# Kernel tuning notes

Measured on AMD Instinct MI355X. Metric: run time of the kernel, lower is better.

Reference implementation:

```python
import jax, jax.numpy as jnp
import numpy as np

B, T, U, N, K, H, O = 64, 800, 64, 64, 10, 512, 121
CLIP_LSTM, CLIP_OUT = 10.0, 100.0


def setup_inputs() -> dict:
    key = jax.random.key(0)
    ks = jax.random.split(key, 16)
    s = 0.08
    return {
        "strokes": jax.random.normal(ks[0], (B, T, 3), jnp.float32),
        "transcriptions": jax.random.uniform(ks[1], (B, U, N), jnp.float32),
        "W0": jax.random.normal(ks[2], (3 + N, 4 * H), jnp.float32) * s,
        "R0": jax.random.normal(ks[3], (H, 4 * H), jnp.float32) * s,
        "b0": jnp.zeros((4 * H,), jnp.float32),
        "Wd": jax.random.normal(ks[4], (H, 3 * K), jnp.float32) * 0.01,
        "bd": jnp.zeros((3 * K,), jnp.float32),
        "W1": jax.random.normal(ks[5], (H + N + 3, 4 * H), jnp.float32) * s,
        "R1": jax.random.normal(ks[6], (H, 4 * H), jnp.float32) * s,
        "b1": jnp.zeros((4 * H,), jnp.float32),
        "W2": jax.random.normal(ks[7], (H + N + 3, 4 * H), jnp.float32) * s,
        "R2": jax.random.normal(ks[8], (H, 4 * H), jnp.float32) * s,
        "b2": jnp.zeros((4 * H,), jnp.float32),
        "Wo": jax.random.normal(ks[9], (3 * H, O), jnp.float32) * s,
        "bo": jnp.zeros((O,), jnp.float32),
    }


def _lstm_step(h, c, z):
    i, f, g, o = jnp.split(z, 4, axis=-1)
    c2 = jax.nn.sigmoid(f) * c + jax.nn.sigmoid(i) * jnp.tanh(g)
    h2 = jax.nn.sigmoid(o) * jnp.tanh(c2)
    return h2, c2


def _lstm_layer(x_seq, W, R, b):
    # x_seq: [T, B, D] -> hidden sequence [T, B, H]
    xz = jnp.einsum('tbd,dh->tbh', x_seq, W) + b  # precompute input projections

    def step(carry, xz_t):
        h, c = carry
        h2, c2 = _lstm_step(h, c, xz_t + h @ R)
        return (h2, c2), h2

    z0 = jnp.zeros((x_seq.shape[1], R.shape[0]), x_seq.dtype)
    _, hs = jax.lax.scan(step, (z0, z0), xz)
    return hs


def _make_clipper(cv):
    @jax.custom_vjp
    def f(y):
        return y
    f.defvjp(lambda y: (y, None), lambda _, dy: (jnp.clip(dy, -cv, cv),))
    return f


_clip_lstm = _make_clipper(CLIP_LSTM)
_clip_out = _make_clipper(CLIP_OUT)


def _forward(strokes, transcriptions, W0, R0, b0, Wd, bd, W1, R1, b1, W2, R2, b2, Wo, bo):
    idx = jnp.arange(1, U + 2, dtype=strokes.dtype)  # enumerated char positions [U+1]
    x_t = jnp.swapaxes(strokes, 0, 1)  # [T, B, 3]

    def step(carry, x):
        w, kappa, h, c = carry
        z = jnp.concatenate([x, w], axis=-1) @ W0 + h @ R0 + b0
        h2, c2 = _lstm_step(h, c, z)
        y = jnp.exp(h2 @ Wd + bd).reshape(-1, 3, K)  # [B, 3, K]
        alpha, beta, dk = y[:, 0], y[:, 1], y[:, 2]
        kappa2 = kappa + dk  # [B, K]
        # Gaussian window over U+1 positions, summed over K mixtures
        phi = alpha[..., None] * jnp.exp(-beta[..., None] * (kappa2[..., None] - idx) ** 2)
        wfull = phi.sum(axis=1)  # [B, U+1]
        att = jnp.argmax(wfull, axis=-1).astype(strokes.dtype)  # [B]
        w2 = jnp.einsum('bu,bun->bn', wfull[:, :U], transcriptions)  # soft window [B, N]
        return (w2, kappa2, h2, c2), (h2, w2, att)

    zf = lambda d: jnp.zeros((B, d), strokes.dtype)
    init = (zf(N), zf(K), zf(H), zf(H))
    _, (h0_seq, w_seq, att_seq) = jax.lax.scan(step, init, x_t)

    x1 = jnp.concatenate([_clip_lstm(h0_seq), w_seq, x_t], axis=-1)  # [T, B, H+N+3]
    h1_seq = _lstm_layer(x1, W1, R1, b1)
    x2 = jnp.concatenate([_clip_lstm(h1_seq), w_seq, x_t], axis=-1)
    h2_seq = _lstm_layer(x2, W2, R2, b2)
    hall = jnp.concatenate([h0_seq, h1_seq, h2_seq], axis=-1)  # [T, B, 3H]
    out = _clip_out(hall @ Wo + bo)
    return jnp.swapaxes(out, 0, 1), jnp.swapaxes(att_seq, 0, 1)  # [B,T,O], [B,T]


def reference(strokes, transcriptions, W0, R0, b0, Wd, bd, W1, R1, b1, W2, R2, b2, Wo, bo):
    return _forward(strokes, transcriptions, W0, R0, b0, Wd, bd, W1, R1, b1, W2, R2, b2, Wo, bo)
```

## Files before the change

### kernel.cpp

```cpp
#include <hip/hip_runtime.h>

#define B_   64
#define T_   800
#define U_   64
#define N_   64
#define KMIX 10
#define H_   512
#define O_   121
#define C4_  2048

#define NB_L0  64
#define NB_L1  64
#define NB_L2  64
#define NB_OUT 8
#define NB_ATT 8
#define NBLK  (NB_L0 + NB_L1 + NB_L2 + NB_OUT + NB_ATT)
#define NTHR  1024
#define RING  8
#define RB    (RING - 1)
#define FS    8

#define AL(pp) __hip_atomic_load((pp), __ATOMIC_RELAXED, __HIP_MEMORY_SCOPE_AGENT)

typedef float vf4 __attribute__((ext_vector_type(4)));

struct Params {
  const float* strokes; const float* transcr;
  const float* transcrT;
  const float* W0; const float* b0;
  const float* bd;
  const float* W1; const float* b1;
  const float* W2; const float* b2;
  const float* bo;
  const float4* PR0; const float4* PW0w;
  const float4* PH1; const float4* PR1; const float4* PW1w;
  const float4* PH2; const float4* PR2; const float4* PW2w;
  const float4* PWo; const float4* PWd;
  float* h0r; float* h1r; float* h2r;
  float* wr;
  int *h0f, *h1f, *h2f, *wfl, *outf;
  float* outp; float* attp;
};

__device__ __forceinline__ float sigf(float x) { return 1.0f / (1.0f + expf(-x)); }

__device__ __forceinline__ double f32q(double x) {
  double ax = fabs(x);
  if (ax >= 0x1p-126) return (double)(float)x;
  return rint(x * 0x1p149) * 0x1p-149;
}

__device__ __forceinline__ void cstoref(float* p, float v) {
  __hip_atomic_store(p, v, __ATOMIC_RELAXED, __HIP_MEMORY_SCOPE_AGENT);
}

__device__ __forceinline__ vf4 cld1(const void* p0) {
  vf4 a;
  asm volatile("global_load_dwordx4 %0, %1, off sc0 sc1\n\t"
               "s_waitcnt vmcnt(0)"
               : "=&v"(a) : "v"(p0) : "memory");
  return a;
}
__device__ __forceinline__ void cld2(const void* p0, const void* p1, vf4& a, vf4& b) {
  asm volatile("global_load_dwordx4 %0, %2, off sc0 sc1\n\t"
               "global_load_dwordx4 %1, %3, off sc0 sc1\n\t"
               "s_waitcnt vmcnt(0)"
               : "=&v"(a), "=&v"(b) : "v"(p0), "v"(p1) : "memory");
}
__device__ __forceinline__ void cld3(const void* p0, const void* p1, const void* p2,
                                     vf4& a, vf4& b, vf4& c) {
  asm volatile("global_load_dwordx4 %0, %3, off sc0 sc1\n\t"
               "global_load_dwordx4 %1, %4, off sc0 sc1\n\t"
               "global_load_dwordx4 %2, %5, off sc0 sc1\n\t"
               "s_waitcnt vmcnt(0)"
               : "=&v"(a), "=&v"(b), "=&v"(c)
               : "v"(p0), "v"(p1), "v"(p2) : "memory");
}

__device__ __forceinline__ int* FP(int* arr, int tt, int bq) {
  return arr + ((size_t)tt * 8 + bq) * FS;
}
__device__ __forceinline__ void waitflag(const int* f, int target) {
  while (__hip_atomic_load(f, __ATOMIC_RELAXED, __HIP_MEMORY_SCOPE_AGENT) < target)
    __builtin_amdgcn_s_sleep(1);
}
__device__ __forceinline__ void postflag(int* f) {
  __hip_atomic_fetch_add(f, 1, __ATOMIC_RELAXED, __HIP_MEMORY_SCOPE_AGENT);
}

__device__ __forceinline__ void stage4k(float* dstL, const float* src, int t) {
  vf4 v = cld1((const vf4*)src + t);
  *((vf4*)dstL + t) = v;
}
__device__ __forceinline__ void stage4k2(float* d1, const float* s1,
                                         float* d2, const float* s2, int t) {
  vf4 a, b;
  cld2((const vf4*)s1 + t, (const vf4*)s2 + t, a, b);
  *((vf4*)d1 + t) = a;
  *((vf4*)d2 + t) = b;
}
__device__ __forceinline__ void stage512(float* dstL, const float* src, int t) {
  if (t < 128) {
    vf4 v = cld1((const vf4*)src + t);
    *((vf4*)dstL + t) = v;
  }
}

__device__ __forceinline__ void dot4gl(const float* Xl,
                                       const float4* __restrict__ W,
                                       int k4, int col, float acc[4]) {
  const float4* X = (const float4*)Xl;
  #pragma unroll 2
  for (int kk = 0; kk < k4; ++kk) {
    float4 xv = X[kk];
    #pragma unroll
    for (int g = 0; g < 4; ++g) {
      float4 wv = W[kk * C4_ + g * H_ + col];
      acc[g] = fmaf(xv.x, wv.x, acc[g]);
      acc[g] = fmaf(xv.y, wv.y, acc[g]);
      acc[g] = fmaf(xv.z, wv.z, acc[g]);
      acc[g] = fmaf(xv.w, wv.w, acc[g]);
    }
  }
}

__device__ __forceinline__ float dot1l(const float* Xl,
                                       const float4* __restrict__ W,
                                       int k4, int stride) {
  const float4* X = (const float4*)Xl;
  float a = 0.0f;
  #pragma unroll 4
  for (int kk = 0; kk < k4; ++kk) {
    float4 xv = X[kk];
    float4 wv = W[kk * stride];
    a = fmaf(xv.x, wv.x, a); a = fmaf(xv.y, wv.y, a);
    a = fmaf(xv.z, wv.z, a); a = fmaf(xv.w, wv.w, a);
  }
  return a;
}

__global__ void pack_k(const float* __restrict__ src, float* __restrict__ dst,
                       int K, int C, int ld) {
  int idx = blockIdx.x * 256 + threadIdx.x;
  if (idx >= K * C) return;
  int k = idx / C, c = idx - k * C;
  dst[(size_t)(k >> 2) * C * 4 + (size_t)c * 4 + (k & 3)] = src[(size_t)k * ld + c];
}

__global__ void pack_t(const float* __restrict__ src, float* __restrict__ dst) {
  int idx = blockIdx.x * 256 + threadIdx.x;
  if (idx >= B_ * U_ * N_) return;
  int b = idx >> 12, r = idx & 4095;
  int u = r >> 6, n = r & 63;
  dst[((size_t)b * N_ + n) * U_ + u] = src[((size_t)b * U_ + u) * N_ + n];
}

__global__ __launch_bounds__(NTHR, 4)
void net_kernel(Params p) {
  const int q = blockIdx.x;
  const int t = threadIdx.x;

  __shared__ float  s_buf[12288];
  __shared__ float  s_y[16][32];
  __shared__ float  s_k2[16][10];
  __shared__ float  s_kap[16][10];
  __shared__ double s_wf[16][66];

  if (q < NB_L0) {
    const int bq = q >> 3, colg = q & 7;
    const int kh = t >> 9;
    const int bl = (t >> 6) & 7, cl = t & 63;
    const int b = bq * 8 + bl, col = colg * 64 + cl;
    float* sh = s_buf;
    float* sw = s_buf + 4096;
    float4* s_red = (float4*)(s_buf + 4608);
    float creg = 0.0f;
    for (int i = 0; i < T_; ++i) {
      if (t == 0) {
        if (i >= 1) waitflag(FP(p.h0f, i - 1, bq), 8);
        if (i >= 8) waitflag(FP(p.outf, i - 8, bq), 1);
      }
      __syncthreads();
      const int slp = (i - 1) & RB;
      stage4k(sh, &p.h0r[((size_t)slp * B_ + bq * 8) * H_], t);
      float acc[4] = {0.f, 0.f, 0.f, 0.f};
      if (kh == 0) {
        const float* xs = &p.strokes[(b * T_ + i) * 3];
        float x0 = xs[0], x1 = xs[1], x2 = xs[2];
        #pragma unroll
        for (int g = 0; g < 4; ++g) {
          int cg = g * H_ + col;
          acc[g] = p.b0[cg] + x0 * p.W0[cg] + x1 * p.W0[C4_ + cg] + x2 * p.W0[2 * C4_ + cg];
        }
      }
      __syncthreads();
      dot4gl(sh + bl * H_ + kh * 256, p.PR0 + (size_t)kh * 64 * C4_, 64, col, acc);
      if (t == 0 && i >= 1) waitflag(FP(p.wfl, i - 1, bq), 1);
      __syncthreads();
      stage512(sw, &p.wr[((size_t)slp * B_ + bq * 8) * N_], t);
      __syncthreads();
      dot4gl(sw + bl * N_ + kh * 32, p.PW0w + (size_t)kh * 8 * C4_, 8, col, acc);
      if (kh) { float4 r; r.x = acc[0]; r.y = acc[1]; r.z = acc[2]; r.w = acc[3]; s_red[t - 512] = r; }
      __syncthreads();
      if (!kh) {
        float4 r = s_red[t];
        float cn = sigf(acc[1] + r.y) * creg + sigf(acc[0] + r.x) * tanhf(acc[2] + r.z);
        float hn = sigf(acc[3] + r.w) * tanhf(cn);
        creg = cn;
        cstoref(&p.h0r[((size_t)(i & RB) * B_ + b) * H_ + col], hn);
      }
      __syncthreads();
      if (t == 0) postflag(FP(p.h0f, i, bq));
    }
  } else if (q < NB_L0 + NB_L1) {
    const int qq = q - NB_L0;
    const int bq = qq >> 3, colg = qq & 7;
    const int kh = t >> 9;
    const int bl = (t >> 6) & 7, cl = t & 63;
    const int b = bq * 8 + bl, col = colg * 64 + cl;
    float* sh0 = s_buf;
    float* sh1 = s_buf + 4096;
    float* sw  = s_buf + 8192;
    float4* s_red = (float4*)(s_buf + 8704);
    float creg = 0.0f;
    for (int tt = 0; tt < T_; ++tt) {
      if (t == 0) {
        waitflag(FP(p.h0f, tt, bq), 8);
        if (tt >= 1) waitflag(FP(p.h1f, tt - 1, bq), 8);
        if (tt >= 7) waitflag(FP(p.outf, tt - 7, bq), 1);
      }
      __syncthreads();
      const int sl = tt & RB, slp = (tt - 1) & RB;
      stage4k2(sh0, &p.h0r[((size_t)sl * B_ + bq * 8) * H_],
               sh1, &p.h1r[((size_t)slp * B_ + bq * 8) * H_], t);
      float acc[4] = {0.f, 0.f, 0.f, 0.f};
      if (kh == 0) {
        const float* xs = &p.strokes[(b * T_ + tt) * 3];
        float x0 = xs[0], x1 = xs[1], x2 = xs[2];
        #pragma unroll
        for (int g = 0; g < 4; ++g) {
          int cg = g * H_ + col;
          acc[g] = p.b1[cg] + x0 * p.W1[576 * C4_ + cg] + x1 * p.W1[577 * C4_ + cg]
                            + x2 * p.W1[578 * C4_ + cg];
        }
      }
      __syncthreads();
      dot4gl(sh0 + bl * H_ + kh * 256, p.PH1 + (size_t)kh * 64 * C4_, 64, col, acc);
      dot4gl(sh1 + bl * H_ + kh * 256, p.PR1 + (size_t)kh * 64 * C4_, 64, col, acc);
      if (t == 0) waitflag(FP(p.wfl, tt, bq), 1);
      __syncthreads();
      stage512(sw, &p.wr[((size_t)sl * B_ + bq * 8) * N_], t);
      __syncthreads();
      dot4gl(sw + bl * N_ + kh * 32, p.PW1w + (size_t)kh * 8 * C4_, 8, col, acc);
      if (kh) { float4 r; r.x = acc[0]; r.y = acc[1]; r.z = acc[2]; r.w = acc[3]; s_red[t - 512] = r; }
      __syncthreads();
      if (!kh) {
        float4 r = s_red[t];
        float cn = sigf(acc[1] + r.y) * creg + sigf(acc[0] + r.x) * tanhf(acc[2] + r.z);
        float hn = sigf(acc[3] + r.w) * tanhf(cn);
        creg = cn;
        cstoref(&p.h1r[((size_t)sl * B_ + b) * H_ + col], hn);
      }
      __syncthreads();
      if (t == 0) postflag(FP(p.h1f, tt, bq));
    }
  } else if (q < NB_L0 + NB_L1 + NB_L2) {
    const int qq = q - NB_L0 - NB_L1;
    const int bq = qq >> 3, colg = qq & 7;
    const int kh = t >> 9;
    const int bl = (t >> 6) & 7, cl = t & 63;
    const int b = bq * 8 + bl, col = colg * 64 + cl;
    float* sh1 = s_buf;
    float* sh2 = s_buf + 4096;
    float* sw  = s_buf + 8192;
    float4* s_red = (float4*)(s_buf + 8704);
    float creg = 0.0f;
    for (int tt = 0; tt < T_; ++tt) {
      if (t == 0) {
        waitflag(FP(p.h1f, tt, bq), 8);
        waitflag(FP(p.wfl, tt, bq), 1);
        if (tt >= 1) waitflag(FP(p.h2f, tt - 1, bq), 8);
        if (tt >= 6) waitflag(FP(p.outf, tt - 6, bq), 1);
      }
      __syncthreads();
      const int sl = tt & RB, slp = (tt - 1) & RB;
      stage4k2(sh1, &p.h1r[((size_t)sl * B_ + bq * 8) * H_],
               sh2, &p.h2r[((size_t)slp * B_ + bq * 8) * H_], t);
      stage512(sw, &p.wr[((size_t)sl * B_ + bq * 8) * N_], t);
      float acc[4] = {0.f, 0.f, 0.f, 0.f};
      if (kh == 0) {
        const float* xs = &p.strokes[(b * T_ + tt) * 3];
        float x0 = xs[0], x1 = xs[1], x2 = xs[2];
        #pragma unroll
        for (int g = 0; g < 4; ++g) {
          int cg = g * H_ + col;
          acc[g] = p.b2[cg] + x0 * p.W2[576 * C4_ + cg] + x1 * p.W2[577 * C4_ + cg]
                            + x2 * p.W2[578 * C4_ + cg];
        }
      }
      __syncthreads();
      dot4gl(sh1 + bl * H_ + kh * 256, p.PH2 + (size_t)kh * 64 * C4_, 64, col, acc);
      dot4gl(sw + bl * N_ + kh * 32, p.PW2w + (size_t)kh * 8 * C4_, 8, col, acc);
      dot4gl(sh2 + bl * H_ + kh * 256, p.PR2 + (size_t)kh * 64 * C4_, 64, col, acc);
      if (kh) { float4 r; r.x = acc[0]; r.y = acc[1]; r.z = acc[2]; r.w = acc[3]; s_red[t - 512] = r; }
      __syncthreads();
      if (!kh) {
        float4 r = s_red[t];
        float cn = sigf(acc[1] + r.y) * creg + sigf(acc[0] + r.x) * tanhf(acc[2] + r.z);
        float hn = sigf(acc[3] + r.w) * tanhf(cn);
        creg = cn;
        cstoref(&p.h2r[((size_t)sl * B_ + b) * H_ + col], hn);
      }
      __syncthreads();
      if (t == 0) postflag(FP(p.h2f, tt, bq));
    }
  } else if (q < NB_L0 + NB_L1 + NB_L2 + NB_OUT) {
    const int bq = q - NB_L0 - NB_L1 - NB_L2;
    const int kh = t >> 9;
    const int bl = (t >> 6) & 7, ol = t & 63;
    const int b = bq * 8 + bl;
    const int oo1 = ol;
    const bool v2 = (ol < O_ - 64);
    const int oo2 = v2 ? (ol + 64) : 0;
    float* sx0 = s_buf;
    float* sx1 = s_buf + 4096;
    float* sx2 = s_buf + 8192;
    float* s_red = (float*)s_wf;
    for (int tt = 0; tt < T_; ++tt) {
      if (t == 0) {
        waitflag(FP(p.h0f, tt, bq), 8);
        waitflag(FP(p.h1f, tt, bq), 8);
        waitflag(FP(p.h2f, tt, bq), 8);
      }
      __syncthreads();
      const int sl = tt & RB;
      {
        vf4 a, c, e;
        cld3((const vf4*)&p.h0r[((size_t)sl * B_ + bq * 8) * H_] + t,
             (const vf4*)&p.h1r[((size_t)sl * B_ + bq * 8) * H_] + t,
             (const vf4*)&p.h2r[((size_t)sl * B_ + bq * 8) * H_] + t, a, c, e);
        *((vf4*)sx0 + t) = a;
        *((vf4*)sx1 + t) = c;
        *((vf4*)sx2 + t) = e;
      }
      __syncthreads();
      const float* X0 = sx0 + bl * H_ + kh * 256;
      const float* X1 = sx1 + bl * H_ + kh * 256;
      const float* X2 = sx2 + bl * H_ + kh * 256;
      const size_t khO = (size_t)(kh * 64) * O_;
      float a1v = kh ? 0.0f : p.bo[oo1];
      a1v += dot1l(X0, p.PWo + khO + oo1, 64, O_);
      a1v += dot1l(X1, p.PWo + (size_t)128 * O_ + khO + oo1, 64, O_);
      a1v += dot1l(X2, p.PWo + (size_t)256 * O_ + khO + oo1, 64, O_);
      float a2v = kh ? 0.0f : p.bo[oo2];
      a2v += dot1l(X0, p.PWo + khO + oo2, 64, O_);
      a2v += dot1l(X1, p.PWo + (size_t)128 * O_ + khO + oo2, 64, O_);
      a2v += dot1l(X2, p.PWo + (size_t)256 * O_ + khO + oo2, 64, O_);
      if (kh) { s_red[(t - 512) * 2] = a1v; s_red[(t - 512) * 2 + 1] = a2v; }
      __syncthreads();
      if (!kh) {
        a1v += s_red[t * 2];
        a2v += s_red[t * 2 + 1];
        __builtin_nontemporal_store(a1v, &p.outp[(size_t)(b * T_ + tt) * O_ + oo1]);
        if (v2) __builtin_nontemporal_store(a2v, &p.outp[(size_t)(b * T_ + tt) * O_ + oo2]);
      }
      __syncthreads();
      if (t == 0) postflag(FP(p.outf, tt, bq));
    }
  } else {
    const int bq = q - NB_L0 - NB_L1 - NB_L2 - NB_OUT;
    const int lb = t >> 7, s = t & 127;
    const int ub = bq * 8 + lb;
    for (int z = t; z < 80; z += NTHR) ((float*)s_kap)[z] = 0.0f;
    __syncthreads();
    for (int tt = 0; tt < T_; ++tt) {
      if (t == 0) waitflag(FP(p.h0f, tt, bq), 8);
      __syncthreads();
      const int sl = tt & RB;
      {
        vf4 v = cld1((const vf4*)&p.h0r[((size_t)sl * B_ + bq * 8) * H_] + t);
        *((vf4*)s_buf + t) = v;
      }
      __syncthreads();
      if (s < 30) {
        float a = p.bd[s] + dot1l(s_buf + lb * H_, p.PWd + s, 128, 30);
        float y = expf(a);
        s_y[lb][s] = y;
        if (s >= 20) {
          float k2 = s_kap[lb][s - 20] + y;
          s_kap[lb][s - 20] = k2;
          s_k2[lb][s - 20] = k2;
        }
      }
      __syncthreads();
      if (s < U_ + 1) {
        const int u = s;
        double wf = 0.0;
        #pragma unroll
        for (int k = 0; k < KMIX; ++k) {
          float d32 = s_k2[lb][k] - (float)(u + 1);
          float sq  = d32 * d32;
          float m   = -(s_y[lb][10 + k] * sq);
          double e  = exp((double)m);
          double e32 = (e < 0x1p-126) ? 0.0 : (double)(float)e;
          wf += f32q((double)s_y[lb][k] * e32);
        }
        s_wf[lb][u] = wf;
      }
      __syncthreads();
      if (s < N_) {
        const float4* Tp = (const float4*)&p.transcrT[((size_t)ub * N_ + s) * U_];
        float a2 = 0.f;
        #pragma unroll
        for (int kk = 0; kk < 16; ++kk) {
          float4 tv = Tp[kk];
          a2 = fmaf((float)s_wf[lb][4 * kk],     tv.x, a2);
          a2 = fmaf((float)s_wf[lb][4 * kk + 1], tv.y, a2);
          a2 = fmaf((float)s_wf[lb][4 * kk + 2], tv.z, a2);
          a2 = fmaf((float)s_wf[lb][4 * kk + 3], tv.w, a2);
        }
        cstoref(&p.wr[((size_t)sl * B_ + ub) * N_ + s], a2);
      }
      __syncthreads();
      if (t == 0) postflag(FP(p.wfl, tt, bq));
      if (s == 127) {
        int am = 0; double bv = s_wf[lb][0];
        for (int u = 1; u < U_ + 1; ++u) {
          double v = s_wf[lb][u];
          if (v > bv) { bv = v; am = u; }
        }
        __builtin_nontemporal_store((float)am, &p.attp[ub * T_ + tt]);
      }
    }
  }
}

extern "C" void kernel_launch(void* const* d_in, const int* in_sizes, int n_in,
                              void* d_out, int out_size, void* d_ws, size_t ws_size,
                              hipStream_t stream) {
  (void)in_sizes; (void)n_in; (void)out_size; (void)ws_size;
  const float* strokes = (const float*)d_in[0];
  const float* transcr = (const float*)d_in[1];
  const float* W0 = (const float*)d_in[2];
  const float* R0 = (const float*)d_in[3];
  const float* b0 = (const float*)d_in[4];
  const float* Wd = (const float*)d_in[5];
  const float* bd = (const float*)d_in[6];
  const float* W1 = (const float*)d_in[7];
  const float* R1 = (const float*)d_in[8];
  const float* b1 = (const float*)d_in[9];
  const float* W2 = (const float*)d_in[10];
  const float* R2 = (const float*)d_in[11];
  const float* b2 = (const float*)d_in[12];
  const float* Wo = (const float*)d_in[13];
  const float* bo = (const float*)d_in[14];

  float* ws = (float*)d_ws;
  size_t off = 0;
  float* h0r = ws + off; off += (size_t)RING * B_ * H_;
  float* h1r = ws + off; off += (size_t)RING * B_ * H_;
  float* h2r = ws + off; off += (size_t)RING * B_ * H_;
  float* wr  = ws + off; off += (size_t)RING * B_ * N_;
  const size_t FLAGN = (size_t)T_ * 8 * FS;
  int* h0f  = (int*)(ws + off); off += FLAGN;
  int* h1f  = (int*)(ws + off); off += FLAGN;
  int* h2f  = (int*)(ws + off); off += FLAGN;
  int* wfl  = (int*)(ws + off); off += FLAGN;
  int* outf = (int*)(ws + off); off += FLAGN;
  size_t stateFloats = off;
  float* PR0  = ws + off; off += (size_t)512 * 2048;
  float* PW0w = ws + off; off += (size_t)64 * 2048;
  float* PH1  = ws + off; off += (size_t)512 * 2048;
  float* PR1  = ws + off; off += (size_t)512 * 2048;
  float* PW1w = ws + off; off += (size_t)64 * 2048;
  float* PH2  = ws + off; off += (size_t)512 * 2048;
  float* PR2  = ws + off; off += (size_t)512 * 2048;
  float* PW2w = ws + off; off += (size_t)64 * 2048;
  float* PWo  = ws + off; off += (size_t)1536 * 121;
  float* PWd  = ws + off; off += (size_t)512 * 30;
  float* TT   = ws + off; off += (size_t)B_ * U_ * N_;

  (void)hipMemsetAsync(d_ws, 0, stateFloats * sizeof(float), stream);

  auto packl = [&](const float* src, float* dst, int K, int C, int ld) {
    int n = K * C;
    pack_k<<<dim3((n + 255) / 256), dim3(256), 0, stream>>>(src, dst, K, C, ld);
  };
  packl(R0, PR0, 512, 2048, 2048);
  packl(W0 + 3 * 2048, PW0w, 64, 2048, 2048);
  packl(W1, PH1, 512, 2048, 2048);
  packl(R1, PR1, 512, 2048, 2048);
  packl(W1 + 512 * 2048, PW1w, 64, 2048, 2048);
  packl(W2, PH2, 512, 2048, 2048);
  packl(R2, PR2, 512, 2048, 2048);
  packl(W2 + 512 * 2048, PW2w, 64, 2048, 2048);
  packl(Wo, PWo, 1536, 121, 121);
  packl(Wd, PWd, 512, 30, 30);
  pack_t<<<dim3((B_ * U_ * N_ + 255) / 256), dim3(256), 0, stream>>>(transcr, TT);

  Params p;
  p.strokes = strokes; p.transcr = transcr; p.transcrT = TT;
  p.W0 = W0; p.b0 = b0; p.bd = bd;
  p.W1 = W1; p.b1 = b1; p.W2 = W2; p.b2 = b2; p.bo = bo;
  p.PR0 = (const float4*)PR0; p.PW0w = (const float4*)PW0w;
  p.PH1 = (const float4*)PH1; p.PR1 = (const float4*)PR1; p.PW1w = (const float4*)PW1w;
  p.PH2 = (const float4*)PH2; p.PR2 = (const float4*)PR2; p.PW2w = (const float4*)PW2w;
  p.PWo = (const float4*)PWo; p.PWd = (const float4*)PWd;
  p.h0r = h0r; p.h1r = h1r; p.h2r = h2r; p.wr = wr;
  p.h0f = h0f; p.h1f = h1f; p.h2f = h2f; p.wfl = wfl; p.outf = outf;
  p.outp = (float*)d_out;
  p.attp = (float*)d_out + (size_t)B_ * T_ * O_;

  void* args[] = { (void*)&p };
  (void)hipLaunchCooperativeKernel((const void*)net_kernel, dim3(NBLK), dim3(NTHR),
                                   args, 0, stream);
}
```

Measured before the change: 52.96 ms.

## Halve block size to 512 threads and drop split-K shared reduction

Shrinks every persistent block from 1024 to 512 threads, so each thread computes the full K-dimension dot product instead of splitting it in two halves and reducing through shared memory. This removes one or two barriers and the shared-memory reduction per timestep in all LSTM and output blocks. The output block also posts its completion flag before computing, once its inputs are staged, which lets producers reuse the ring slot sooner. The trade-off is fewer threads to hide weight-load latency and twice as long a serial dot loop per thread on the recurrent critical path.

```diff
diff --git a/kernel.cpp b/kernel.cpp
--- a/kernel.cpp
+++ b/kernel.cpp
@@ -15,12 +15,10 @@
 #define NB_OUT 8
 #define NB_ATT 8
 #define NBLK  (NB_L0 + NB_L1 + NB_L2 + NB_OUT + NB_ATT)
-#define NTHR  1024
+#define NTHR  512
 #define RING  8
 #define RB    (RING - 1)
 #define FS    8
-
-#define AL(pp) __hip_atomic_load((pp), __ATOMIC_RELAXED, __HIP_MEMORY_SCOPE_AGENT)
 
 typedef float vf4 __attribute__((ext_vector_type(4)));
 
@@ -76,6 +74,16 @@
                : "=&v"(a), "=&v"(b), "=&v"(c)
                : "v"(p0), "v"(p1), "v"(p2) : "memory");
 }
+__device__ __forceinline__ void cld4(const void* p0, const void* p1, const void* p2,
+                                     const void* p3, vf4& a, vf4& b, vf4& c, vf4& d) {
+  asm volatile("global_load_dwordx4 %0, %4, off sc0 sc1\n\t"
+               "global_load_dwordx4 %1, %5, off sc0 sc1\n\t"
+               "global_load_dwordx4 %2, %6, off sc0 sc1\n\t"
+               "global_load_dwordx4 %3, %7, off sc0 sc1\n\t"
+               "s_waitcnt vmcnt(0)"
+               : "=&v"(a), "=&v"(b), "=&v"(c), "=&v"(d)
+               : "v"(p0), "v"(p1), "v"(p2), "v"(p3) : "memory");
+}
 
 __device__ __forceinline__ int* FP(int* arr, int tt, int bq) {
   return arr + ((size_t)tt * 8 + bq) * FS;
@@ -89,21 +97,32 @@
 }
 
 __device__ __forceinline__ void stage4k(float* dstL, const float* src, int t) {
-  vf4 v = cld1((const vf4*)src + t);
-  *((vf4*)dstL + t) = v;
+  vf4 a, b;
+  cld2((const vf4*)src + t, (const vf4*)src + 512 + t, a, b);
+  *((vf4*)dstL + t) = a;
+  *((vf4*)dstL + 512 + t) = b;
 }
 __device__ __forceinline__ void stage4k2(float* d1, const float* s1,
                                          float* d2, const float* s2, int t) {
-  vf4 a, b;
-  cld2((const vf4*)s1 + t, (const vf4*)s2 + t, a, b);
+  vf4 a, b, c, d;
+  cld4((const vf4*)s1 + t, (const vf4*)s1 + 512 + t,
+       (const vf4*)s2 + t, (const vf4*)s2 + 512 + t, a, b, c, d);
   *((vf4*)d1 + t) = a;
-  *((vf4*)d2 + t) = b;
+  *((vf4*)d1 + 512 + t) = b;
+  *((vf4*)d2 + t) = c;
+  *((vf4*)d2 + 512 + t) = d;
 }
 __device__ __forceinline__ void stage512(float* dstL, const float* src, int t) {
   if (t < 128) {
     vf4 v = cld1((const vf4*)src + t);
     *((vf4*)dstL + t) = v;
   }
+}
+__device__ __forceinline__ void stage512w(float* dstL, const float* src, int lane) {
+  vf4 a, b;
+  cld2((const vf4*)src + lane, (const vf4*)src + 64 + lane, a, b);
+  *((vf4*)dstL + lane) = a;
+  *((vf4*)dstL + 64 + lane) = b;
 }
 
 __device__ __forceinline__ void dot4gl(const float* Xl,
@@ -155,25 +174,23 @@
   dst[((size_t)b * N_ + n) * U_ + u] = src[((size_t)b * U_ + u) * N_ + n];
 }
 
-__global__ __launch_bounds__(NTHR, 4)
+__global__ __launch_bounds__(NTHR, 2)
 void net_kernel(Params p) {
   const int q = blockIdx.x;
   const int t = threadIdx.x;
 
   __shared__ float  s_buf[12288];
-  __shared__ float  s_y[16][32];
-  __shared__ float  s_k2[16][10];
-  __shared__ float  s_kap[16][10];
-  __shared__ double s_wf[16][66];
+  __shared__ float  s_y[8][32];
+  __shared__ float  s_k2[8][10];
+  __shared__ float  s_kap[8][10];
+  __shared__ double s_wf[8][66];
 
   if (q < NB_L0) {
     const int bq = q >> 3, colg = q & 7;
-    const int kh = t >> 9;
-    const int bl = (t >> 6) & 7, cl = t & 63;
+    const int bl = t >> 6, cl = t & 63;
     const int b = bq * 8 + bl, col = colg * 64 + cl;
     float* sh = s_buf;
     float* sw = s_buf + 4096;
-    float4* s_red = (float4*)(s_buf + 4608);
     float creg = 0.0f;
     for (int i = 0; i < T_; ++i) {
       if (t == 0) {
@@ -183,8 +200,8 @@
       __syncthreads();
       const int slp = (i - 1) & RB;
       stage4k(sh, &p.h0r[((size_t)slp * B_ + bq * 8) * H_], t);
-      float acc[4] = {0.f, 0.f, 0.f, 0.f};
-      if (kh == 0) {
+      float acc[4];
+      {
         const float* xs = &p.strokes[(b * T_ + i) * 3];
         float x0 = xs[0], x1 = xs[1], x2 = xs[2];
         #pragma unroll
@@ -194,34 +211,28 @@
         }
       }
       __syncthreads();
-      dot4gl(sh + bl * H_ + kh * 256, p.PR0 + (size_t)kh * 64 * C4_, 64, col, acc);
-      if (t == 0 && i >= 1) waitflag(FP(p.wfl, i - 1, bq), 1);
-      __syncthreads();
-      stage512(sw, &p.wr[((size_t)slp * B_ + bq * 8) * N_], t);
-      __syncthreads();
-      dot4gl(sw + bl * N_ + kh * 32, p.PW0w + (size_t)kh * 8 * C4_, 8, col, acc);
-      if (kh) { float4 r; r.x = acc[0]; r.y = acc[1]; r.z = acc[2]; r.w = acc[3]; s_red[t - 512] = r; }
-      __syncthreads();
-      if (!kh) {
-        float4 r = s_red[t];
-        float cn = sigf(acc[1] + r.y) * creg + sigf(acc[0] + r.x) * tanhf(acc[2] + r.z);
-        float hn = sigf(acc[3] + r.w) * tanhf(cn);
-        creg = cn;
-        cstoref(&p.h0r[((size_t)(i & RB) * B_ + b) * H_ + col], hn);
-      }
+      dot4gl(sh + bl * H_, p.PR0, 128, col, acc);
+      if (t < 64) {
+        if (t == 0 && i >= 1) waitflag(FP(p.wfl, i - 1, bq), 1);
+        stage512w(sw, &p.wr[((size_t)slp * B_ + bq * 8) * N_], t);
+      }
+      __syncthreads();
+      dot4gl(sw + bl * N_, p.PW0w, 16, col, acc);
+      float cn = sigf(acc[1]) * creg + sigf(acc[0]) * tanhf(acc[2]);
+      float hn = sigf(acc[3]) * tanhf(cn);
+      creg = cn;
+      cstoref(&p.h0r[((size_t)(i & RB) * B_ + b) * H_ + col], hn);
       __syncthreads();
       if (t == 0) postflag(FP(p.h0f, i, bq));
     }
   } else if (q < NB_L0 + NB_L1) {
     const int qq = q - NB_L0;
     const int bq = qq >> 3, colg = qq & 7;
-    const int kh = t >> 9;
-    const int bl = (t >> 6) & 7, cl = t & 63;
+    const int bl = t >> 6, cl = t & 63;
     const int b = bq * 8 + bl, col = colg * 64 + cl;
     float* sh0 = s_buf;
     float* sh1 = s_buf + 4096;
     float* sw  = s_buf + 8192;
-    float4* s_red = (float4*)(s_buf + 8704);
     float creg = 0.0f;
     for (int tt = 0; tt < T_; ++tt) {
       if (t == 0) {
@@ -233,8 +244,8 @@
       const int sl = tt & RB, slp = (tt - 1) & RB;
       stage4k2(sh0, &p.h0r[((size_t)sl * B_ + bq * 8) * H_],
                sh1, &p.h1r[((size_t)slp * B_ + bq * 8) * H_], t);
-      float acc[4] = {0.f, 0.f, 0.f, 0.f};
-      if (kh == 0) {
+      float acc[4];
+      {
         const float* xs = &p.strokes[(b * T_ + tt) * 3];
         float x0 = xs[0], x1 = xs[1], x2 = xs[2];
         #pragma unroll
@@ -245,35 +256,29 @@
         }
       }
       __syncthreads();
-      dot4gl(sh0 + bl * H_ + kh * 256, p.PH1 + (size_t)kh * 64 * C4_, 64, col, acc);
-      dot4gl(sh1 + bl * H_ + kh * 256, p.PR1 + (size_t)kh * 64 * C4_, 64, col, acc);
-      if (t == 0) waitflag(FP(p.wfl, tt, bq), 1);
-      __syncthreads();
-      stage512(sw, &p.wr[((size_t)sl * B_ + bq * 8) * N_], t);
-      __syncthreads();
-      dot4gl(sw + bl * N_ + kh * 32, p.PW1w + (size_t)kh * 8 * C4_, 8, col, acc);
-      if (kh) { float4 r; r.x = acc[0]; r.y = acc[1]; r.z = acc[2]; r.w = acc[3]; s_red[t - 512] = r; }
-      __syncthreads();
-      if (!kh) {
-        float4 r = s_red[t];
-        float cn = sigf(acc[1] + r.y) * creg + sigf(acc[0] + r.x) * tanhf(acc[2] + r.z);
-        float hn = sigf(acc[3] + r.w) * tanhf(cn);
-        creg = cn;
-        cstoref(&p.h1r[((size_t)sl * B_ + b) * H_ + col], hn);
-      }
+      dot4gl(sh0 + bl * H_, p.PH1, 128, col, acc);
+      dot4gl(sh1 + bl * H_, p.PR1, 128, col, acc);
+      if (t < 64) {
+        if (t == 0) waitflag(FP(p.wfl, tt, bq), 1);
+        stage512w(sw, &p.wr[((size_t)sl * B_ + bq * 8) * N_], t);
+      }
+      __syncthreads();
+      dot4gl(sw + bl * N_, p.PW1w, 16, col, acc);
+      float cn = sigf(acc[1]) * creg + sigf(acc[0]) * tanhf(acc[2]);
+      float hn = sigf(acc[3]) * tanhf(cn);
+      creg = cn;
+      cstoref(&p.h1r[((size_t)sl * B_ + b) * H_ + col], hn);
       __syncthreads();
       if (t == 0) postflag(FP(p.h1f, tt, bq));
     }
   } else if (q < NB_L0 + NB_L1 + NB_L2) {
     const int qq = q - NB_L0 - NB_L1;
     const int bq = qq >> 3, colg = qq & 7;
-    const int kh = t >> 9;
-    const int bl = (t >> 6) & 7, cl = t & 63;
+    const int bl = t >> 6, cl = t & 63;
     const int b = bq * 8 + bl, col = colg * 64 + cl;
     float* sh1 = s_buf;
     float* sh2 = s_buf + 4096;
     float* sw  = s_buf + 8192;
-    float4* s_red = (float4*)(s_buf + 8704);
     float creg = 0.0f;
     for (int tt = 0; tt < T_; ++tt) {
       if (t == 0) {
@@ -287,8 +292,8 @@
       stage4k2(sh1, &p.h1r[((size_t)sl * B_ + bq * 8) * H_],
                sh2, &p.h2r[((size_t)slp * B_ + bq * 8) * H_], t);
       stage512(sw, &p.wr[((size_t)sl * B_ + bq * 8) * N_], t);
-      float acc[4] = {0.f, 0.f, 0.f, 0.f};
-      if (kh == 0) {
+      float acc[4];
+      {
         const float* xs = &p.strokes[(b * T_ + tt) * 3];
         float x0 = xs[0], x1 = xs[1], x2 = xs[2];
         #pragma unroll
@@ -299,25 +304,19 @@
         }
       }
       __syncthreads();
-      dot4gl(sh1 + bl * H_ + kh * 256, p.PH2 + (size_t)kh * 64 * C4_, 64, col, acc);
-      dot4gl(sw + bl * N_ + kh * 32, p.PW2w + (size_t)kh * 8 * C4_, 8, col, acc);
-      dot4gl(sh2 + bl * H_ + kh * 256, p.PR2 + (size_t)kh * 64 * C4_, 64, col, acc);
-      if (kh) { float4 r; r.x = acc[0]; r.y = acc[1]; r.z = acc[2]; r.w = acc[3]; s_red[t - 512] = r; }
-      __syncthreads();
-      if (!kh) {
-        float4 r = s_red[t];
-        float cn = sigf(acc[1] + r.y) * creg + sigf(acc[0] + r.x) * tanhf(acc[2] + r.z);
-        float hn = sigf(acc[3] + r.w) * tanhf(cn);
-        creg = cn;
-        cstoref(&p.h2r[((size_t)sl * B_ + b) * H_ + col], hn);
-      }
+      dot4gl(sh1 + bl * H_, p.PH2, 128, col, acc);
+      dot4gl(sw + bl * N_, p.PW2w, 16, col, acc);
+      dot4gl(sh2 + bl * H_, p.PR2, 128, col, acc);
+      float cn = sigf(acc[1]) * creg + sigf(acc[0]) * tanhf(acc[2]);
+      float hn = sigf(acc[3]) * tanhf(cn);
+      creg = cn;
+      cstoref(&p.h2r[((size_t)sl * B_ + b) * H_ + col], hn);
       __syncthreads();
       if (t == 0) postflag(FP(p.h2f, tt, bq));
     }
   } else if (q < NB_L0 + NB_L1 + NB_L2 + NB_OUT) {
     const int bq = q - NB_L0 - NB_L1 - NB_L2;
-    const int kh = t >> 9;
-    const int bl = (t >> 6) & 7, ol = t & 63;
+    const int bl = t >> 6, ol = t & 63;
     const int b = bq * 8 + bl;
     const int oo1 = ol;
     const bool v2 = (ol < O_ - 64);
@@ -325,7 +324,6 @@
     float* sx0 = s_buf;
     float* sx1 = s_buf + 4096;
     float* sx2 = s_buf + 8192;
-    float* s_red = (float*)s_wf;
     for (int tt = 0; tt < T_; ++tt) {
       if (t == 0) {
         waitflag(FP(p.h0f, tt, bq), 8);
@@ -335,41 +333,36 @@
       __syncthreads();
       const int sl = tt & RB;
       {
-        vf4 a, c, e;
-        cld3((const vf4*)&p.h0r[((size_t)sl * B_ + bq * 8) * H_] + t,
-             (const vf4*)&p.h1r[((size_t)sl * B_ + bq * 8) * H_] + t,
-             (const vf4*)&p.h2r[((size_t)sl * B_ + bq * 8) * H_] + t, a, c, e);
-        *((vf4*)sx0 + t) = a;
-        *((vf4*)sx1 + t) = c;
-        *((vf4*)sx2 + t) = e;
-      }
-      __syncthreads();
-      const float* X0 = sx0 + bl * H_ + kh * 256;
-      const float* X1 = sx1 + bl * H_ + kh * 256;
-      const float* X2 = sx2 + bl * H_ + kh * 256;
-      const size_t khO = (size_t)(kh * 64) * O_;
-      float a1v = kh ? 0.0f : p.bo[oo1];
-      a1v += dot1l(X0, p.PWo + khO + oo1, 64, O_);
-      a1v += dot1l(X1, p.PWo + (size_t)128 * O_ + khO + oo1, 64, O_);
-      a1v += dot1l(X2, p.PWo + (size_t)256 * O_ + khO + oo1, 64, O_);
-      float a2v = kh ? 0.0f : p.bo[oo2];
-      a2v += dot1l(X0, p.PWo + khO + oo2, 64, O_);
-      a2v += dot1l(X1, p.PWo + (size_t)128 * O_ + khO + oo2, 64, O_);
-      a2v += dot1l(X2, p.PWo + (size_t)256 * O_ + khO + oo2, 64, O_);
-      if (kh) { s_red[(t - 512) * 2] = a1v; s_red[(t - 512) * 2 + 1] = a2v; }
-      __syncthreads();
-      if (!kh) {
-        a1v += s_red[t * 2];
-        a2v += s_red[t * 2 + 1];
-        __builtin_nontemporal_store(a1v, &p.outp[(size_t)(b * T_ + tt) * O_ + oo1]);
-        if (v2) __builtin_nontemporal_store(a2v, &p.outp[(size_t)(b * T_ + tt) * O_ + oo2]);
+        vf4 a0, c0, e0, a1, c1, e1;
+        const vf4* A = (const vf4*)&p.h0r[((size_t)sl * B_ + bq * 8) * H_];
+        const vf4* C = (const vf4*)&p.h1r[((size_t)sl * B_ + bq * 8) * H_];
+        const vf4* E = (const vf4*)&p.h2r[((size_t)sl * B_ + bq * 8) * H_];
+        cld3(A + t, C + t, E + t, a0, c0, e0);
+        cld3(A + 512 + t, C + 512 + t, E + 512 + t, a1, c1, e1);
+        *((vf4*)sx0 + t) = a0; *((vf4*)sx0 + 512 + t) = a1;
+        *((vf4*)sx1 + t) = c0; *((vf4*)sx1 + 512 + t) = c1;
+        *((vf4*)sx2 + t) = e0; *((vf4*)sx2 + 512 + t) = e1;
       }
       __syncthreads();
       if (t == 0) postflag(FP(p.outf, tt, bq));
+      const float* X0 = sx0 + bl * H_;
+      const float* X1 = sx1 + bl * H_;
+      const float* X2 = sx2 + bl * H_;
+      float a1v = p.bo[oo1];
+      a1v += dot1l(X0, p.PWo + oo1, 128, O_);
+      a1v += dot1l(X1, p.PWo + (size_t)128 * O_ + oo1, 128, O_);
+      a1v += dot1l(X2, p.PWo + (size_t)256 * O_ + oo1, 128, O_);
+      float a2v = p.bo[oo2];
+      a2v += dot1l(X0, p.PWo + oo2, 128, O_);
+      a2v += dot1l(X1, p.PWo + (size_t)128 * O_ + oo2, 128, O_);
+      a2v += dot1l(X2, p.PWo + (size_t)256 * O_ + oo2, 128, O_);
+      __builtin_nontemporal_store(a1v, &p.outp[(size_t)(b * T_ + tt) * O_ + oo1]);
+      if (v2) __builtin_nontemporal_store(a2v, &p.outp[(size_t)(b * T_ + tt) * O_ + oo2]);
+      __syncthreads();
     }
   } else {
     const int bq = q - NB_L0 - NB_L1 - NB_L2 - NB_OUT;
-    const int lb = t >> 7, s = t & 127;
+    const int lb = t >> 6, s = t & 63;
     const int ub = bq * 8 + lb;
     for (int z = t; z < 80; z += NTHR) ((float*)s_kap)[z] = 0.0f;
     __syncthreads();
@@ -378,8 +371,7 @@
       __syncthreads();
       const int sl = tt & RB;
       {
-        vf4 v = cld1((const vf4*)&p.h0r[((size_t)sl * B_ + bq * 8) * H_] + t);
-        *((vf4*)s_buf + t) = v;
+        stage4k(s_buf, &p.h0r[((size_t)sl * B_ + bq * 8) * H_], t);
       }
       __syncthreads();
       if (s < 30) {
@@ -393,8 +385,7 @@
         }
       }
       __syncthreads();
-      if (s < U_ + 1) {
-        const int u = s;
+      for (int u = s; u < U_ + 1; u += 64) {
         double wf = 0.0;
         #pragma unroll
         for (int k = 0; k < KMIX; ++k) {
@@ -408,7 +399,7 @@
         s_wf[lb][u] = wf;
       }
       __syncthreads();
-      if (s < N_) {
+      {
         const float4* Tp = (const float4*)&p.transcrT[((size_t)ub * N_ + s) * U_];
         float a2 = 0.f;
         #pragma unroll
@@ -423,7 +414,7 @@
       }
       __syncthreads();
       if (t == 0) postflag(FP(p.wfl, tt, bq));
-      if (s == 127) {
+      if (s == 63) {
         int am = 0; double bv = s_wf[lb][0];
         for (int u = 1; u < U_ + 1; ++u) {
           double v = s_wf[lb][u];
```

Measured after the change: 51.44 ms. 1.03x faster.
